# Optimization experiments

Hardware: AMD Instinct MI355X
Metric: run time of the kernel (lower is better)

## Reference

```python
import jax, jax.numpy as jnp
import numpy as np

D_MODEL = 1024
NUM_HEADS = 16
D_K = D_MODEL // NUM_HEADS


def setup_inputs() -> dict:
    key = jax.random.key(0)
    ks = jax.random.split(key, 11)
    B, S = 1, 4096
    s = 1.0 / np.sqrt(D_MODEL)
    return {
        "query": jax.random.normal(ks[0], (B, S, D_MODEL), jnp.float32),
        "key": jax.random.normal(ks[1], (B, S, D_MODEL), jnp.float32),
        "value": jax.random.normal(ks[2], (B, S, D_MODEL), jnp.float32),
        "Wq": jax.random.normal(ks[3], (D_MODEL, D_MODEL), jnp.float32) * s,
        "bq": jnp.zeros((D_MODEL,), jnp.float32),
        "Wk": jax.random.normal(ks[4], (D_MODEL, D_MODEL), jnp.float32) * s,
        "bk": jnp.zeros((D_MODEL,), jnp.float32),
        "Wv": jax.random.normal(ks[5], (D_MODEL, D_MODEL), jnp.float32) * s,
        "bv": jnp.zeros((D_MODEL,), jnp.float32),
        "Wo": jax.random.normal(ks[6], (D_MODEL, D_MODEL), jnp.float32) * s,
        "bo": jnp.zeros((D_MODEL,), jnp.float32),
    }


def reference(query, key, value, Wq, bq, Wk, bk, Wv, bv, Wo, bo):
    B, S, _ = query.shape
    # linear projections, split into heads: [B, H, S, d_k]
    def proj(x, W, b):
        y = x @ W.T + b
        return y.reshape(B, -1, NUM_HEADS, D_K).transpose(0, 2, 1, 3)

    q = proj(query, Wq, bq)
    k = proj(key, Wk, bk)
    v = proj(value, Wv, bv)

    scale = D_K ** (-0.5)
    scores = jnp.einsum("bhqd,bhkd->bhqk", q, k) * scale  # [B,H,S,S]
    attn = jax.nn.softmax(scores, axis=-1)
    out = jnp.einsum("bhqk,bhkd->bhqd", attn, v)  # [B,H,S,d_k]
    out = out.transpose(0, 2, 1, 3).reshape(B, -1, NUM_HEADS * D_K)
    return out @ Wo.T + bo
```

## Files before the change

### kernel.cpp

```cpp
#include <hip/hip_runtime.h>

typedef __bf16 bf16;
typedef __bf16 bf16x8 __attribute__((ext_vector_type(8)));
typedef float floatx4 __attribute__((ext_vector_type(4)));

#define MFMA(a, b, c) __builtin_amdgcn_mfma_f32_16x16x32_bf16((a), (b), (c), 0, 0, 0)

__device__ inline bf16x8 load8(const bf16* p) { return *(const bf16x8*)(p); }

__device__ inline void store_c(bf16* p, float v) { *p = (bf16)v; }
__device__ inline void store_c(float* p, float v) { *p = v; }

__device__ inline void gload_lds(const bf16* g, bf16* l) {
    __builtin_amdgcn_global_load_lds(
        (const __attribute__((address_space(1))) void*)(g),
        (__attribute__((address_space(3))) void*)(l), 16, 0, 0);
}

struct CvtArgs {
    const float* src[7];
    bf16* dst[7];
    int n[7];
};
__global__ __launch_bounds__(256) void cvt_bf16(CvtArgs a) {
    const int t = blockIdx.y;
    const int i = (blockIdx.x * 256 + threadIdx.x) * 8;
    if (i >= a.n[t]) return;
    const float4 u = *(const float4*)(a.src[t] + i);
    const float4 v = *(const float4*)(a.src[t] + i + 4);
    bf16x8 r;
    r[0] = (bf16)u.x; r[1] = (bf16)u.y; r[2] = (bf16)u.z; r[3] = (bf16)u.w;
    r[4] = (bf16)v.x; r[5] = (bf16)v.y; r[6] = (bf16)v.z; r[7] = (bf16)v.w;
    *(bf16x8*)(a.dst[t] + i) = r;
}

template <typename TC>
__device__ inline void gemm_core(const bf16* __restrict__ A, const bf16* __restrict__ W,
                                 const float* __restrict__ bias, TC* __restrict__ C,
                                 bool TR) {
    __shared__ bf16 As[2][128][32];
    __shared__ bf16 Bs[2][128][32];

    const int tid = threadIdx.x;
    const int wv = tid >> 6, lane = tid & 63;
    const int quad = lane >> 4, lo = lane & 15;
    const int wm = wv >> 1, wn = wv & 1;
    const int Ar0 = blockIdx.y * 128, Br0 = blockIdx.x * 128;

    const int srow = lane >> 2, sseg = (lane & 3) ^ (srow & 3);
    const bf16* Ag = A + (size_t)(Ar0 + srow) * 1024 + sseg * 8;
    const bf16* Bg = W + (size_t)(Br0 + srow) * 1024 + sseg * 8;

    auto stage = [&](int buf, int k0) {
#pragma unroll
        for (int c = 2 * wv; c < 2 * wv + 2; c++) {
            gload_lds(Ag + (size_t)c * 16 * 1024 + k0, &As[buf][c * 16][0]);
            gload_lds(Bg + (size_t)c * 16 * 1024 + k0, &Bs[buf][c * 16][0]);
        }
    };

    floatx4 acc[4][4] = {};
    const int rs = (quad ^ (lo & 3)) * 8;

    stage(0, 0);
    for (int k0 = 0; k0 < 1024; k0 += 32) {
        const int buf = (k0 >> 5) & 1;
        __syncthreads();
        if (k0 + 32 < 1024) stage(buf ^ 1, k0 + 32);

        bf16x8 a[4], b[4];
#pragma unroll
        for (int i = 0; i < 4; i++) a[i] = load8(&As[buf][wm * 64 + i * 16 + lo][rs]);
#pragma unroll
        for (int j = 0; j < 4; j++) b[j] = load8(&Bs[buf][wn * 64 + j * 16 + lo][rs]);
#pragma unroll
        for (int i = 0; i < 4; i++)
#pragma unroll
            for (int j = 0; j < 4; j++) acc[i][j] = MFMA(a[i], b[j], acc[i][j]);
    }

#pragma unroll
    for (int i = 0; i < 4; i++) {
#pragma unroll
        for (int j = 0; j < 4; j++) {
#pragma unroll
            for (int r = 0; r < 4; r++) {
                const int m = Ar0 + wm * 64 + i * 16 + quad * 4 + r;
                const int n = Br0 + wn * 64 + j * 16 + lo;
                const float v = acc[i][j][r] + bias[n];
                if (!TR) {
                    store_c(C + (size_t)m * 1024 + n, v);
                } else {
                    store_c(C + (size_t)(n >> 6) * (64 * 4096) + (size_t)(n & 63) * 4096 + m, v);
                }
            }
        }
    }
}

__global__ __launch_bounds__(256) void gemm_qkv(
    const bf16* __restrict__ qb, const bf16* __restrict__ kb, const bf16* __restrict__ vb,
    const bf16* __restrict__ Wq, const bf16* __restrict__ Wk, const bf16* __restrict__ Wv,
    const float* __restrict__ bq, const float* __restrict__ bk, const float* __restrict__ bv,
    bf16* __restrict__ Q, bf16* __restrict__ Kp, bf16* __restrict__ Vt) {
    if (blockIdx.z == 0)
        gemm_core<bf16>(qb, Wq, bq, Q, false);
    else if (blockIdx.z == 1)
        gemm_core<bf16>(kb, Wk, bk, Kp, false);
    else
        gemm_core<bf16>(vb, Wv, bv, Vt, true);
}

__global__ __launch_bounds__(256) void gemm_o(const bf16* __restrict__ O,
                                              const bf16* __restrict__ Wo,
                                              const float* __restrict__ bo,
                                              float* __restrict__ out) {
    gemm_core<float>(O, Wo, bo, out, false);
}

__global__ __launch_bounds__(256) void flash_attn3(const bf16* __restrict__ Q,
                                                   const bf16* __restrict__ Kmat,
                                                   const bf16* __restrict__ Vt,
                                                   bf16* __restrict__ O) {
    __shared__ bf16 Ks[2][64][64];
    __shared__ bf16 Vs[2][64][64];
    __shared__ bf16 Ps[4][2][16][72];

    const int tid = threadIdx.x;
    const int wv = tid >> 6;
    const int lane = tid & 63;
    const int quad = lane >> 4, lo = lane & 15;
    const int h = blockIdx.x;
    const int qb = blockIdx.y;
    const int DM = 1024;
    const int q0 = qb * 128 + wv * 32;

    bf16x8 aQ[2][2];
#pragma unroll
    for (int qs = 0; qs < 2; qs++) {
        const bf16* qp = Q + (size_t)(q0 + qs * 16 + lo) * DM + h * 64 + quad * 8;
        aQ[qs][0] = load8(qp);
        aQ[qs][1] = load8(qp + 32);
    }

    floatx4 Oacc[2][4] = {};
    float lsum[2][4] = {{0.f}};

    const int srow = lane >> 3, sseg = (lane & 7) ^ srow;
    const bf16* Kg = Kmat + (size_t)srow * DM + h * 64 + sseg * 8;
    const bf16* Vg = Vt + (size_t)h * 64 * 4096 + (size_t)srow * 4096 + sseg * 8;

    auto stage = [&](int buf, int kb2) {
#pragma unroll
        for (int c = 2 * wv; c < 2 * wv + 2; c++) {
            gload_lds(Kg + (size_t)(kb2 + c * 8) * DM, &Ks[buf][c * 8][0]);
            gload_lds(Vg + (size_t)(c * 8) * 4096 + kb2, &Vs[buf][c * 8][0]);
        }
    };

    const float C_SCALE = 0.18033688011112043f;
    const float C_BIAS = 23.083120654223415f;
    const int sw = lo & 7;

    stage(0, 0);
    for (int kb2 = 0; kb2 < 4096; kb2 += 64) {
        const int buf = (kb2 >> 6) & 1;
        __syncthreads();
        if (kb2 + 64 < 4096) stage(buf ^ 1, kb2 + 64);

        floatx4 sc[2][4];
#pragma unroll
        for (int t = 0; t < 4; t++) {
            const bf16* krow = &Ks[buf][t * 16 + lo][0];
            const bf16x8 b0 = load8(krow + ((quad ^ sw) * 8));
            const bf16x8 b1 = load8(krow + (((quad + 4) ^ sw) * 8));
#pragma unroll
            for (int qs = 0; qs < 2; qs++) {
                floatx4 z = {};
                z = MFMA(aQ[qs][0], b0, z);
                sc[qs][t] = MFMA(aQ[qs][1], b1, z);
            }
        }

#pragma unroll
        for (int qs = 0; qs < 2; qs++)
#pragma unroll
            for (int t = 0; t < 4; t++)
#pragma unroll
                for (int r = 0; r < 4; r++) {
                    const float p = exp2f(fmaf(sc[qs][t][r], C_SCALE, -C_BIAS));
                    const bf16 pb = (bf16)p;
                    lsum[qs][r] += (float)pb;
                    Ps[wv][qs][quad * 4 + r][t * 16 + lo] = pb;
                }

#pragma unroll
        for (int kk = 0; kk < 2; kk++) {
            bf16x8 aP[2];
            aP[0] = load8(&Ps[wv][0][lo][kk * 32 + quad * 8]);
            aP[1] = load8(&Ps[wv][1][lo][kk * 32 + quad * 8]);
#pragma unroll
            for (int nt = 0; nt < 4; nt++) {
                const bf16x8 bV = load8(&Vs[buf][nt * 16 + lo][(((kk * 4 + quad) ^ sw) * 8)]);
                Oacc[0][nt] = MFMA(aP[0], bV, Oacc[0][nt]);
                Oacc[1][nt] = MFMA(aP[1], bV, Oacc[1][nt]);
            }
        }
    }

#pragma unroll
    for (int qs = 0; qs < 2; qs++)
#pragma unroll
        for (int r = 0; r < 4; r++) {
            float v = lsum[qs][r];
#pragma unroll
            for (int m = 1; m < 16; m <<= 1) v += __shfl_xor(v, m, 64);
            lsum[qs][r] = v;
        }
#pragma unroll
    for (int qs = 0; qs < 2; qs++)
#pragma unroll
        for (int nt = 0; nt < 4; nt++)
#pragma unroll
            for (int r = 0; r < 4; r++) {
                O[(size_t)(q0 + qs * 16 + quad * 4 + r) * DM + h * 64 + nt * 16 + lo] =
                    (bf16)(Oacc[qs][nt][r] / lsum[qs][r]);
            }
}

extern "C" void kernel_launch(void* const* d_in, const int* in_sizes, int n_in,
                              void* d_out, int out_size, void* d_ws, size_t ws_size,
                              hipStream_t stream) {
    const float* query = (const float*)d_in[0];
    const float* key_i = (const float*)d_in[1];
    const float* value = (const float*)d_in[2];
    const float* Wq = (const float*)d_in[3];
    const float* bq = (const float*)d_in[4];
    const float* Wk = (const float*)d_in[5];
    const float* bk = (const float*)d_in[6];
    const float* Wv = (const float*)d_in[7];
    const float* bv = (const float*)d_in[8];
    const float* Wo = (const float*)d_in[9];
    const float* bo = (const float*)d_in[10];

    bf16* ws = (bf16*)d_ws;
    const size_t SZ = (size_t)4096 * 1024;
    const size_t WZ = (size_t)1024 * 1024;
    bf16* qb = ws;
    bf16* kb = ws + SZ;
    bf16* vb = ws + 2 * SZ;
    bf16* Wqb = ws + 3 * SZ;
    bf16* Wkb = ws + 3 * SZ + WZ;
    bf16* Wvb = ws + 3 * SZ + 2 * WZ;
    bf16* Wob = ws + 3 * SZ + 3 * WZ;
    bf16* Q = ws + 3 * SZ + 4 * WZ;
    bf16* K = Q + SZ;
    bf16* Vt = Q + 2 * SZ;
    bf16* O = qb;

    CvtArgs ca;
    ca.src[0] = query; ca.dst[0] = qb;  ca.n[0] = (int)SZ;
    ca.src[1] = key_i; ca.dst[1] = kb;  ca.n[1] = (int)SZ;
    ca.src[2] = value; ca.dst[2] = vb;  ca.n[2] = (int)SZ;
    ca.src[3] = Wq;    ca.dst[3] = Wqb; ca.n[3] = (int)WZ;
    ca.src[4] = Wk;    ca.dst[4] = Wkb; ca.n[4] = (int)WZ;
    ca.src[5] = Wv;    ca.dst[5] = Wvb; ca.n[5] = (int)WZ;
    ca.src[6] = Wo;    ca.dst[6] = Wob; ca.n[6] = (int)WZ;
    cvt_bf16<<<dim3(2048, 7), 256, 0, stream>>>(ca);

    gemm_qkv<<<dim3(8, 32, 3), 256, 0, stream>>>(qb, kb, vb, Wqb, Wkb, Wvb,
                                                 bq, bk, bv, Q, K, Vt);
    flash_attn3<<<dim3(16, 32), 256, 0, stream>>>(Q, K, Vt, O);
    gemm_o<<<dim3(8, 32), 256, 0, stream>>>(O, Wob, bo, (float*)d_out);
}
```

Before: 318.3 us.

## Split attention key range across two blocks with atomic accumulation and normalize pass

The attention kernel now splits the 4096-key range into two halves via a third grid dimension. Each half atomically adds its unnormalized fp32 output and row sums into a zeroed workspace, and a new kernel divides and converts to bf16 before the output projection. This doubles block count to improve CU occupancy and load balance. In exchange it adds a memset, fp32 atomic traffic and an extra normalization kernel.

```diff
diff --git a/kernel.cpp b/kernel.cpp
--- a/kernel.cpp
+++ b/kernel.cpp
@@ -2,6 +2,7 @@
 
 typedef __bf16 bf16;
 typedef __bf16 bf16x8 __attribute__((ext_vector_type(8)));
+typedef __bf16 bf16x4 __attribute__((ext_vector_type(4)));
 typedef float floatx4 __attribute__((ext_vector_type(4)));
 
 #define MFMA(a, b, c) __builtin_amdgcn_mfma_f32_16x16x32_bf16((a), (b), (c), 0, 0, 0)
@@ -118,10 +119,11 @@
     gemm_core<float>(O, Wo, bo, out, false);
 }
 
-__global__ __launch_bounds__(256) void flash_attn3(const bf16* __restrict__ Q,
+__global__ __launch_bounds__(256) void flash_attn4(const bf16* __restrict__ Q,
                                                    const bf16* __restrict__ Kmat,
                                                    const bf16* __restrict__ Vt,
-                                                   bf16* __restrict__ O) {
+                                                   float* __restrict__ Of,
+                                                   float* __restrict__ Lf) {
     __shared__ bf16 Ks[2][64][64];
     __shared__ bf16 Vs[2][64][64];
     __shared__ bf16 Ps[4][2][16][72];
@@ -132,6 +134,7 @@
     const int quad = lane >> 4, lo = lane & 15;
     const int h = blockIdx.x;
     const int qb = blockIdx.y;
+    const int split = blockIdx.z;
     const int DM = 1024;
     const int q0 = qb * 128 + wv * 32;
 
@@ -162,11 +165,12 @@
     const float C_BIAS = 23.083120654223415f;
     const int sw = lo & 7;
 
-    stage(0, 0);
-    for (int kb2 = 0; kb2 < 4096; kb2 += 64) {
+    const int kbeg = split * 2048, kend = kbeg + 2048;
+    stage(0, kbeg);
+    for (int kb2 = kbeg; kb2 < kend; kb2 += 64) {
         const int buf = (kb2 >> 6) & 1;
         __syncthreads();
-        if (kb2 + 64 < 4096) stage(buf ^ 1, kb2 + 64);
+        if (kb2 + 64 < kend) stage(buf ^ 1, kb2 + 64);
 
         floatx4 sc[2][4];
 #pragma unroll
@@ -189,9 +193,8 @@
 #pragma unroll
                 for (int r = 0; r < 4; r++) {
                     const float p = exp2f(fmaf(sc[qs][t][r], C_SCALE, -C_BIAS));
-                    const bf16 pb = (bf16)p;
-                    lsum[qs][r] += (float)pb;
-                    Ps[wv][qs][quad * 4 + r][t * 16 + lo] = pb;
+                    lsum[qs][r] += p;
+                    Ps[wv][qs][quad * 4 + r][t * 16 + lo] = (bf16)p;
                 }
 
 #pragma unroll
@@ -217,15 +220,37 @@
             for (int m = 1; m < 16; m <<= 1) v += __shfl_xor(v, m, 64);
             lsum[qs][r] = v;
         }
+
 #pragma unroll
     for (int qs = 0; qs < 2; qs++)
 #pragma unroll
         for (int nt = 0; nt < 4; nt++)
 #pragma unroll
             for (int r = 0; r < 4; r++) {
-                O[(size_t)(q0 + qs * 16 + quad * 4 + r) * DM + h * 64 + nt * 16 + lo] =
-                    (bf16)(Oacc[qs][nt][r] / lsum[qs][r]);
+                const int q = q0 + qs * 16 + quad * 4 + r;
+                atomicAdd(&Of[(size_t)q * DM + h * 64 + nt * 16 + lo], Oacc[qs][nt][r]);
             }
+    if (lo == 0) {
+#pragma unroll
+        for (int qs = 0; qs < 2; qs++)
+#pragma unroll
+            for (int r = 0; r < 4; r++)
+                atomicAdd(&Lf[h * 4096 + q0 + qs * 16 + quad * 4 + r], lsum[qs][r]);
+    }
+}
+
+__global__ __launch_bounds__(256) void normalize(const float* __restrict__ Of,
+                                                 const float* __restrict__ Lf,
+                                                 bf16* __restrict__ Ob) {
+    const int q = blockIdx.x;
+    const int t = threadIdx.x;
+    const int h = t >> 4;
+    const float inv = 1.0f / Lf[h * 4096 + q];
+    const float4 v = ((const float4*)(Of + (size_t)q * 1024))[t];
+    bf16x4 r;
+    r[0] = (bf16)(v.x * inv); r[1] = (bf16)(v.y * inv);
+    r[2] = (bf16)(v.z * inv); r[3] = (bf16)(v.w * inv);
+    ((bf16x4*)(Ob + (size_t)q * 1024))[t] = r;
 }
 
 extern "C" void kernel_launch(void* const* d_in, const int* in_sizes, int n_in,
@@ -243,33 +268,38 @@
     const float* Wo = (const float*)d_in[9];
     const float* bo = (const float*)d_in[10];
 
-    bf16* ws = (bf16*)d_ws;
-    const size_t SZ = (size_t)4096 * 1024;
-    const size_t WZ = (size_t)1024 * 1024;
-    bf16* qb = ws;
-    bf16* kb = ws + SZ;
-    bf16* vb = ws + 2 * SZ;
-    bf16* Wqb = ws + 3 * SZ;
-    bf16* Wkb = ws + 3 * SZ + WZ;
-    bf16* Wvb = ws + 3 * SZ + 2 * WZ;
-    bf16* Wob = ws + 3 * SZ + 3 * WZ;
-    bf16* Q = ws + 3 * SZ + 4 * WZ;
-    bf16* K = Q + SZ;
-    bf16* Vt = Q + 2 * SZ;
-    bf16* O = qb;
+    char* base = (char*)d_ws;
+    const size_t MB = 1 << 20;
+    bf16* qb  = (bf16*)(base);
+    bf16* kb  = (bf16*)(base + 8 * MB);
+    bf16* vb  = (bf16*)(base + 16 * MB);
+    bf16* Wqb = (bf16*)(base + 24 * MB);
+    bf16* Wkb = (bf16*)(base + 26 * MB);
+    bf16* Wvb = (bf16*)(base + 28 * MB);
+    bf16* Wob = (bf16*)(base + 30 * MB);
+    bf16* Q   = (bf16*)(base + 32 * MB);
+    bf16* K   = (bf16*)(base + 40 * MB);
+    bf16* Vt  = (bf16*)(base + 48 * MB);
+    float* Of = (float*)(base);
+    float* Lf = (float*)(base + 16 * MB);
+    bf16* Ob  = (bf16*)(base + 17 * MB);
 
     CvtArgs ca;
-    ca.src[0] = query; ca.dst[0] = qb;  ca.n[0] = (int)SZ;
-    ca.src[1] = key_i; ca.dst[1] = kb;  ca.n[1] = (int)SZ;
-    ca.src[2] = value; ca.dst[2] = vb;  ca.n[2] = (int)SZ;
-    ca.src[3] = Wq;    ca.dst[3] = Wqb; ca.n[3] = (int)WZ;
-    ca.src[4] = Wk;    ca.dst[4] = Wkb; ca.n[4] = (int)WZ;
-    ca.src[5] = Wv;    ca.dst[5] = Wvb; ca.n[5] = (int)WZ;
-    ca.src[6] = Wo;    ca.dst[6] = Wob; ca.n[6] = (int)WZ;
+    const int SZ = 4096 * 1024, WZ = 1024 * 1024;
+    ca.src[0] = query; ca.dst[0] = qb;  ca.n[0] = SZ;
+    ca.src[1] = key_i; ca.dst[1] = kb;  ca.n[1] = SZ;
+    ca.src[2] = value; ca.dst[2] = vb;  ca.n[2] = SZ;
+    ca.src[3] = Wq;    ca.dst[3] = Wqb; ca.n[3] = WZ;
+    ca.src[4] = Wk;    ca.dst[4] = Wkb; ca.n[4] = WZ;
+    ca.src[5] = Wv;    ca.dst[5] = Wvb; ca.n[5] = WZ;
+    ca.src[6] = Wo;    ca.dst[6] = Wob; ca.n[6] = WZ;
     cvt_bf16<<<dim3(2048, 7), 256, 0, stream>>>(ca);
 
     gemm_qkv<<<dim3(8, 32, 3), 256, 0, stream>>>(qb, kb, vb, Wqb, Wkb, Wvb,
                                                  bq, bk, bv, Q, K, Vt);
-    flash_attn3<<<dim3(16, 32), 256, 0, stream>>>(Q, K, Vt, O);
-    gemm_o<<<dim3(8, 32), 256, 0, stream>>>(O, Wob, bo, (float*)d_out);
-}
+    hipMemsetAsync(base, 0, 16 * MB + 4096 * 16 * sizeof(float), stream);
+
+    flash_attn4<<<dim3(16, 32, 2), 256, 0, stream>>>(Q, K, Vt, Of, Lf);
+    normalize<<<4096, 256, 0, stream>>>(Of, Lf, Ob);
+    gemm_o<<<dim3(8, 32), 256, 0, stream>>>(Ob, Wob, bo, (float*)d_out);
+}
```

New measurement: 330.2 us. +3.7%, slower.
